# Optimization experiments

Hardware: AMD Instinct MI355X
Metric: run time of the kernel (lower is better)

## Reference

```python
import jax, jax.numpy as jnp
import numpy as np

B, V, FN, C = 8, 50000, 100000, 64


def setup_inputs() -> dict:
    key = jax.random.key(0)
    keys = iter(jax.random.split(key, 16))
    inp = {}
    inp["centers"] = jax.random.normal(next(keys), (B, 3, FN), jnp.float32)
    inp["verts"] = jax.random.normal(next(keys), (B, V, 3), jnp.float32)
    inp["faces"] = jax.random.randint(next(keys), (B, FN, 3), 0, V)

    def bn(p):
        inp[p + "g"] = jnp.ones((C,), jnp.float32)
        inp[p + "bt"] = jnp.zeros((C,), jnp.float32)
        inp[p + "m"] = jnp.zeros((C,), jnp.float32)
        inp[p + "v"] = jnp.ones((C,), jnp.float32)

    inp["cw1"] = jax.random.normal(next(keys), (C, 3), jnp.float32) * 0.1
    inp["cb1"] = jnp.zeros((C,), jnp.float32); bn("c1")
    inp["cw2"] = jax.random.normal(next(keys), (C, C), jnp.float32) * 0.1
    inp["cb2"] = jnp.zeros((C,), jnp.float32); bn("c2")
    inp["vw1"] = jax.random.normal(next(keys), (C, 6), jnp.float32) * 0.1
    inp["vb1"] = jnp.zeros((C,), jnp.float32); bn("v1")
    inp["vw2"] = jax.random.normal(next(keys), (C, C), jnp.float32) * 0.1
    inp["vb2"] = jnp.zeros((C,), jnp.float32); bn("v2")
    inp["sw"] = jax.random.normal(next(keys), (C, 2 * C), jnp.float32) * 0.1
    inp["sb"] = jnp.zeros((C,), jnp.float32); bn("s1")
    return inp


def _cbr(x, w, b, g, bt, m, v, eps=1e-5):
    # 1x1 Conv1d == pointwise GEMM over channel dim, then eval-mode BN, then ReLU
    y = jnp.einsum('bcf,oc->bof', x, w) + b[:, None]
    y = (y - m[:, None]) * (g[:, None] / jnp.sqrt(v[:, None] + eps)) + bt[:, None]
    return jax.nn.relu(y)


def _forward(faces, centers, verts,
             cw1, cb1, c1g, c1bt, c1m, c1v, cw2, cb2, c2g, c2bt, c2m, c2v,
             vw1, vb1, v1g, v1bt, v1m, v1v, vw2, vb2, v2g, v2bt, v2m, v2v,
             sw, sb, s1g, s1bt, s1m, s1v):
    Bb, Fn, _ = faces.shape
    # gather 3 corner vertices per face: [B, 3F, 3] -> [B, 9, F] (v0xyz, v1xyz, v2xyz)
    idx = faces.reshape(Bb, Fn * 3)
    corners = jnp.take_along_axis(verts, idx[:, :, None], axis=1)
    c9 = corners.reshape(Bb, Fn, 9).transpose(0, 2, 1)

    def vmlp(x):
        return _cbr(_cbr(x, vw1, vb1, v1g, v1bt, v1m, v1v), vw2, vb2, v2g, v2bt, v2m, v2v)

    vfeat = (vmlp(c9[:, :6])
             + vmlp(c9[:, 3:9])
             + vmlp(jnp.concatenate([c9[:, 6:9], c9[:, :3]], axis=1))) / 3.0
    cfeat = _cbr(_cbr(centers, cw1, cb1, c1g, c1bt, c1m, c1v), cw2, cb2, c2g, c2bt, c2m, c2v)
    return _cbr(jnp.concatenate([cfeat, vfeat], axis=1), sw, sb, s1g, s1bt, s1m, s1v)


def reference(centers, verts, faces,
              cw1, cb1, c1g, c1bt, c1m, c1v, cw2, cb2, c2g, c2bt, c2m, c2v,
              vw1, vb1, v1g, v1bt, v1m, v1v, vw2, vb2, v2g, v2bt, v2m, v2v,
              sw, sb, s1g, s1bt, s1m, s1v):
    return _forward(faces, centers, verts,
                    cw1, cb1, c1g, c1bt, c1m, c1v, cw2, cb2, c2g, c2bt, c2m, c2v,
                    vw1, vb1, v1g, v1bt, v1m, v1v, vw2, vb2, v2g, v2bt, v2m, v2v,
                    sw, sb, s1g, s1bt, s1m, s1v)
```

## Files before the change

### kernel.cpp

```cpp
#include <hip/hip_runtime.h>
#include <cstddef>
#include <cstdint>

#define FN_ 100000
#define V_  50000
#define B_  8
#define NT  128
#define NBLK (B_ * FN_ / NT)

#define WS_SHS 49152

typedef _Float16 f16;
typedef f16   f16x8 __attribute__((ext_vector_type(8)));
typedef float f32x4 __attribute__((ext_vector_type(4)));

struct Ptrs { const void* p[33]; };

union Pk4 { f16 h[4]; uint2 u; };
union Pk8 { f16 h[8]; uint4 u; };

__global__ __launch_bounds__(1024) void sd_prep(Ptrs in, f16* __restrict__ wsW,
                                                float* __restrict__ shsG)
{
  const float* __restrict__ cw1 = (const float*)in.p[3];
  const float* __restrict__ cb1 = (const float*)in.p[4];
  const float* __restrict__ c1g = (const float*)in.p[5];
  const float* __restrict__ c1bt= (const float*)in.p[6];
  const float* __restrict__ c1m = (const float*)in.p[7];
  const float* __restrict__ c1v = (const float*)in.p[8];
  const float* __restrict__ cw2 = (const float*)in.p[9];
  const float* __restrict__ cb2 = (const float*)in.p[10];
  const float* __restrict__ c2g = (const float*)in.p[11];
  const float* __restrict__ c2bt= (const float*)in.p[12];
  const float* __restrict__ c2m = (const float*)in.p[13];
  const float* __restrict__ c2v = (const float*)in.p[14];
  const float* __restrict__ vw1 = (const float*)in.p[15];
  const float* __restrict__ vb1 = (const float*)in.p[16];
  const float* __restrict__ v1g = (const float*)in.p[17];
  const float* __restrict__ v1bt= (const float*)in.p[18];
  const float* __restrict__ v1m = (const float*)in.p[19];
  const float* __restrict__ v1v = (const float*)in.p[20];
  const float* __restrict__ vw2 = (const float*)in.p[21];
  const float* __restrict__ vb2 = (const float*)in.p[22];
  const float* __restrict__ v2g = (const float*)in.p[23];
  const float* __restrict__ v2bt= (const float*)in.p[24];
  const float* __restrict__ v2m = (const float*)in.p[25];
  const float* __restrict__ v2v = (const float*)in.p[26];
  const float* __restrict__ sw  = (const float*)in.p[27];
  const float* __restrict__ sb  = (const float*)in.p[28];
  const float* __restrict__ s1g = (const float*)in.p[29];
  const float* __restrict__ s1bt= (const float*)in.p[30];
  const float* __restrict__ s1m = (const float*)in.p[31];
  const float* __restrict__ s1v = (const float*)in.p[32];

  __shared__ float scsL[448];
  const int tid = threadIdx.x;

  if (tid < 448) {
    const float *g, *v, *bb, *m, *bt; int o; float mul = 1.f;
    if (tid < 64)       { o = tid;      g=c1g; v=c1v; bb=cb1; m=c1m; bt=c1bt; }
    else if (tid < 256) { o = tid & 63; g=v1g; v=v1v; bb=vb1; m=v1m; bt=v1bt; }
    else if (tid < 320) { o = tid-256;  g=c2g; v=c2v; bb=cb2; m=c2m; bt=c2bt; }
    else if (tid < 384) { o = tid-320;  g=v2g; v=v2v; bb=vb2; m=v2m; bt=v2bt; mul = 1.f/3.f; }
    else                { o = tid-384;  g=s1g; v=s1v; bb=sb;  m=s1m; bt=s1bt; }
    float s = g[o] * rsqrtf(v[o] + 1e-5f);
    scsL[tid] = s * mul;
    shsG[tid] = ((bb[o] - m[o]) * s + bt[o]) * mul;
  }
  __syncthreads();

  for (int u = tid; u < 3072; u += 1024) {
    const int t = u >> 6, l = u & 63, r15 = l & 15, g4 = l >> 4;
    Pk8 pk;
    if (t < 16) {
      const int wm = t >> 2, tr = t & 3, row = 64*wm + 16*tr + r15;
#pragma unroll
      for (int j = 0; j < 8; ++j) {
        const int k = 8*g4 + j; float val = 0.f;
        if (wm == 0) { if (k >= 9 && k < 12) val = cw1[row*3 + (k-9)]; }
        else if (k < 9) {
          const int e = wm - 1, o = row - 64*wm, c = (k - 3*e + 9) % 9;
          if (c < 6) val = vw1[o*6 + c];
        }
        pk.h[j] = (f16)(val * scsL[row]);
      }
    } else if (t < 24) {
      const int tt = t-16, rt = tt >> 1, s = tt & 1, row = 16*rt + r15;
#pragma unroll
      for (int j = 0; j < 8; ++j) { const int k = 32*s + 8*g4 + j;
        pk.h[j] = (f16)(cw2[row*64 + k] * scsL[256+row]); }
    } else if (t < 32) {
      const int tt = t-24, rt = tt >> 1, s = tt & 1, row = 16*rt + r15;
#pragma unroll
      for (int j = 0; j < 8; ++j) { const int k = 32*s + 8*g4 + j;
        pk.h[j] = (f16)(vw2[row*64 + k] * scsL[320+row]); }
    } else {
      const int tt = t-32, rt = tt >> 2, s = tt & 3, row = 16*rt + r15;
#pragma unroll
      for (int j = 0; j < 8; ++j) { const int k = 32*s + 8*g4 + j;
        pk.h[j] = (f16)(sw[row*128 + k] * scsL[384+row]); }
    }
    *(uint4*)(wsW + (size_t)t*512 + l*8) = pk.u;
  }
}

__global__ __launch_bounds__(512, 4) void sd_main(const int* __restrict__ faces,
    const float* __restrict__ verts, const float* __restrict__ centers,
    const f16* __restrict__ wsW, const float* __restrict__ shsG,
    float* __restrict__ out)
{
  __shared__ f16 Hs[NT][296];
  __shared__ float shsL[448];

  const int tid  = threadIdx.x;
  const int lane = tid & 63;
  const int r15  = lane & 15;
  const int g4   = lane >> 4;
  const int wid  = __builtin_amdgcn_readfirstlane(tid >> 6);

  if (tid < 448) shsL[tid] = shsG[tid];

  {
    const int col = tid >> 2, p = tid & 3;
    const unsigned colg = blockIdx.x * (unsigned)NT + (unsigned)col;
    const unsigned b = colg / FN_;
    const unsigned f = colg - b * FN_;
    if (p < 3) {
      const int vi = faces[(size_t)colg*3 + p];
      const float* vp = verts + ((size_t)b*V_ + (size_t)vi)*3;
      Hs[col][256 + p*3 + 0] = (f16)vp[0];
      Hs[col][256 + p*3 + 1] = (f16)vp[1];
      Hs[col][256 + p*3 + 2] = (f16)vp[2];
    } else {
#pragma unroll
      for (int k = 0; k < 3; ++k)
        Hs[col][265 + k] = (f16)centers[((size_t)b*3 + k)*FN_ + f];
    }
#pragma unroll
    for (int z = 0; z < 5; ++z) Hs[col][268 + p*5 + z] = (f16)0.f;
  }
  __syncthreads();

  const int wm2 = wid >> 2, wn2 = wid & 3;

  f16x8 w2c[2][2], w2v[2][2];
#pragma unroll
  for (int tr = 0; tr < 2; ++tr)
#pragma unroll
    for (int s = 0; s < 2; ++s) {
      w2c[tr][s] = *(const f16x8*)(wsW + (size_t)(16 + (2*wm2+tr)*2 + s)*512 + lane*8);
      w2v[tr][s] = *(const f16x8*)(wsW + (size_t)(24 + (2*wm2+tr)*2 + s)*512 + lane*8);
    }

  {
    const int wm = wid >> 1, wn = wid & 1;
    f16x8 bfr[4];
#pragma unroll
    for (int tc = 0; tc < 4; ++tc)
      bfr[tc] = *(const f16x8*)&Hs[64*wn + 16*tc + r15][256 + 8*g4];
#pragma unroll
    for (int tr = 0; tr < 4; ++tr) {
      const f16x8 a = *(const f16x8*)(wsW + (size_t)(wm*4 + tr)*512 + lane*8);
#pragma unroll
      for (int tc = 0; tc < 4; ++tc) {
        f32x4 acc = {0.f,0.f,0.f,0.f};
        acc = __builtin_amdgcn_mfma_f32_16x16x32_f16(a, bfr[tc], acc, 0,0,0);
        const int o0  = 64*wm + 16*tr + 4*g4;
        const int col = 64*wn + 16*tc + r15;
        const f32x4 sh = *(const f32x4*)&shsL[o0];
        Pk4 pk;
#pragma unroll
        for (int j = 0; j < 4; ++j) pk.h[j] = (f16)fmaxf(acc[j] + sh[j], 0.f);
        *(uint2*)&Hs[col][o0] = pk.u;
      }
    }
  }
  __syncthreads();

  float cf[2][2][4], vf[2][2][4];
#pragma unroll
  for (int tr = 0; tr < 2; ++tr)
#pragma unroll
    for (int tc = 0; tc < 2; ++tc)
#pragma unroll
      for (int j = 0; j < 4; ++j) vf[tr][tc][j] = 0.f;

#pragma unroll
  for (int br = 0; br < 4; ++br) {
    f32x4 acc[2][2];
#pragma unroll
    for (int tr = 0; tr < 2; ++tr)
#pragma unroll
      for (int tc = 0; tc < 2; ++tc) acc[tr][tc] = (f32x4){0.f,0.f,0.f,0.f};
#pragma unroll
    for (int s = 0; s < 2; ++s) {
      const f16x8 b0 = *(const f16x8*)&Hs[32*wn2 +      r15][64*br + 32*s + 8*g4];
      const f16x8 b1 = *(const f16x8*)&Hs[32*wn2 + 16 + r15][64*br + 32*s + 8*g4];
#pragma unroll
      for (int tr = 0; tr < 2; ++tr) {
        const f16x8 a = br ? w2v[tr][s] : w2c[tr][s];
        acc[tr][0] = __builtin_amdgcn_mfma_f32_16x16x32_f16(a, b0, acc[tr][0], 0,0,0);
        acc[tr][1] = __builtin_amdgcn_mfma_f32_16x16x32_f16(a, b1, acc[tr][1], 0,0,0);
      }
    }
#pragma unroll
    for (int tr = 0; tr < 2; ++tr) {
      const int o0 = 32*wm2 + 16*tr + 4*g4;
      const f32x4 sh = br ? *(const f32x4*)&shsL[320+o0] : *(const f32x4*)&shsL[256+o0];
#pragma unroll
      for (int tc = 0; tc < 2; ++tc)
#pragma unroll
        for (int j = 0; j < 4; ++j) {
          if (br == 0) cf[tr][tc][j]  = fmaxf(acc[tr][tc][j] + sh[j], 0.f);
          else         vf[tr][tc][j] += fmaxf(acc[tr][tc][j] + sh[j], 0.f);
        }
    }
  }
  __syncthreads();

#pragma unroll
  for (int tr = 0; tr < 2; ++tr)
#pragma unroll
    for (int tc = 0; tc < 2; ++tc) {
      const int o0  = 32*wm2 + 16*tr + 4*g4;
      const int col = 32*wn2 + 16*tc + r15;
      Pk4 pc, pv;
#pragma unroll
      for (int j = 0; j < 4; ++j) { pc.h[j] = (f16)cf[tr][tc][j]; pv.h[j] = (f16)vf[tr][tc][j]; }
      *(uint2*)&Hs[col][o0]      = pc.u;
      *(uint2*)&Hs[col][64 + o0] = pv.u;
    }
  __syncthreads();

  {
    f32x4 acc[2][2];
#pragma unroll
    for (int tr = 0; tr < 2; ++tr)
#pragma unroll
      for (int tc = 0; tc < 2; ++tc) acc[tr][tc] = (f32x4){0.f,0.f,0.f,0.f};
#pragma unroll
    for (int s = 0; s < 4; ++s) {
      const f16x8 b0 = *(const f16x8*)&Hs[32*wn2 +      r15][32*s + 8*g4];
      const f16x8 b1 = *(const f16x8*)&Hs[32*wn2 + 16 + r15][32*s + 8*g4];
#pragma unroll
      for (int tr = 0; tr < 2; ++tr) {
        const f16x8 a = *(const f16x8*)(wsW + (size_t)(32 + (2*wm2+tr)*4 + s)*512 + lane*8);
        acc[tr][0] = __builtin_amdgcn_mfma_f32_16x16x32_f16(a, b0, acc[tr][0], 0,0,0);
        acc[tr][1] = __builtin_amdgcn_mfma_f32_16x16x32_f16(a, b1, acc[tr][1], 0,0,0);
      }
    }
#pragma unroll
    for (int tr = 0; tr < 2; ++tr)
#pragma unroll
      for (int tc = 0; tc < 2; ++tc) {
        const unsigned colg = blockIdx.x * (unsigned)NT + 32*wn2 + 16*tc + r15;
        const unsigned b = colg / FN_;
        const unsigned f = colg - b * FN_;
        const int o0 = 32*wm2 + 16*tr + 4*g4;
        const f32x4 sh = *(const f32x4*)&shsL[384 + o0];
#pragma unroll
        for (int j = 0; j < 4; ++j)
          out[((size_t)(b*64u + o0 + j))*FN_ + f] = fmaxf(acc[tr][tc][j] + sh[j], 0.f);
      }
  }
}

extern "C" void kernel_launch(void* const* d_in, const int* in_sizes, int n_in,
                              void* d_out, int out_size, void* d_ws, size_t ws_size,
                              hipStream_t stream) {
  (void)in_sizes; (void)n_in; (void)out_size; (void)ws_size;
  Ptrs p;
  for (int i = 0; i < 33; ++i) p.p[i] = d_in[i];
  f16*   wsW  = (f16*)d_ws;
  float* shsG = (float*)((char*)d_ws + WS_SHS);
  hipLaunchKernelGGL(sd_prep, dim3(1), dim3(1024), 0, stream, p, wsW, shsG);
  hipLaunchKernelGGL(sd_main, dim3(NBLK), dim3(512), 0, stream,
                     (const int*)d_in[2], (const float*)d_in[1], (const float*)d_in[0],
                     wsW, shsG, (float*)d_out);
}
```

Baseline: 98.02 us.

## Split layer-1 into two halves to shrink LDS tile and raise occupancy

Computes the first layer (64 centre channels plus 192 vertex channels) in two 128-row halves, each followed by its layer-2 GEMMs, so the shared-memory tile shrinks from 296 to 168 halves per column. Launch bounds rise to 6 waves per SIMD. The grid becomes 2D (face blocks by batch), which removes the per-column divide and handles the tail with bounds checks. Bias is folded into the MFMA accumulator init, and warps are remapped so each covers 16 rows by 64 columns. In exchange there are extra barriers and more register pressure from holding 4x4 accumulators.

```diff
diff --git a/kernel.cpp b/kernel.cpp
--- a/kernel.cpp
+++ b/kernel.cpp
@@ -6,7 +6,7 @@
 #define V_  50000
 #define B_  8
 #define NT  128
-#define NBLK (B_ * FN_ / NT)
+#define NBX 782
 
 #define WS_SHS 49152
 
@@ -104,12 +104,12 @@
   }
 }
 
-__global__ __launch_bounds__(512, 4) void sd_main(const int* __restrict__ faces,
+__global__ __launch_bounds__(512, 6) void sd_main(const int* __restrict__ faces,
     const float* __restrict__ verts, const float* __restrict__ centers,
     const f16* __restrict__ wsW, const float* __restrict__ shsG,
     float* __restrict__ out)
 {
-  __shared__ f16 Hs[NT][296];
+  __shared__ f16 Hs[NT][168];
   __shared__ float shsL[448];
 
   const int tid  = threadIdx.x;
@@ -117,151 +117,147 @@
   const int r15  = lane & 15;
   const int g4   = lane >> 4;
   const int wid  = __builtin_amdgcn_readfirstlane(tid >> 6);
+  const int rt   = wid & 3;
+  const int cg   = wid >> 2;
+
+  const int by   = blockIdx.y;
+  const int col0 = blockIdx.x * NT;
 
   if (tid < 448) shsL[tid] = shsG[tid];
 
   {
     const int col = tid >> 2, p = tid & 3;
-    const unsigned colg = blockIdx.x * (unsigned)NT + (unsigned)col;
-    const unsigned b = colg / FN_;
-    const unsigned f = colg - b * FN_;
+    const int f = col0 + col;
+    const bool valid = f < FN_;
     if (p < 3) {
-      const int vi = faces[(size_t)colg*3 + p];
-      const float* vp = verts + ((size_t)b*V_ + (size_t)vi)*3;
-      Hs[col][256 + p*3 + 0] = (f16)vp[0];
-      Hs[col][256 + p*3 + 1] = (f16)vp[1];
-      Hs[col][256 + p*3 + 2] = (f16)vp[2];
+      float x0 = 0.f, x1 = 0.f, x2 = 0.f;
+      if (valid) {
+        const int vi = faces[((size_t)by*FN_ + f)*3 + p];
+        const float* vp = verts + ((size_t)by*V_ + (size_t)vi)*3;
+        x0 = vp[0]; x1 = vp[1]; x2 = vp[2];
+      }
+      Hs[col][128 + p*3 + 0] = (f16)x0;
+      Hs[col][128 + p*3 + 1] = (f16)x1;
+      Hs[col][128 + p*3 + 2] = (f16)x2;
     } else {
 #pragma unroll
       for (int k = 0; k < 3; ++k)
-        Hs[col][265 + k] = (f16)centers[((size_t)b*3 + k)*FN_ + f];
-    }
-#pragma unroll
-    for (int z = 0; z < 5; ++z) Hs[col][268 + p*5 + z] = (f16)0.f;
+        Hs[col][137 + k] = valid ? (f16)centers[((size_t)by*3 + k)*FN_ + f] : (f16)0.f;
+    }
+#pragma unroll
+    for (int z = 0; z < 5; ++z) Hs[col][140 + p*5 + z] = (f16)0.f;
   }
   __syncthreads();
 
-  const int wm2 = wid >> 2, wn2 = wid & 3;
-
-  f16x8 w2c[2][2], w2v[2][2];
-#pragma unroll
-  for (int tr = 0; tr < 2; ++tr)
-#pragma unroll
-    for (int s = 0; s < 2; ++s) {
-      w2c[tr][s] = *(const f16x8*)(wsW + (size_t)(16 + (2*wm2+tr)*2 + s)*512 + lane*8);
-      w2v[tr][s] = *(const f16x8*)(wsW + (size_t)(24 + (2*wm2+tr)*2 + s)*512 + lane*8);
-    }
+  float cf[4][4], vf[4][4];
+  f16x8 w2v[2];
+
+#pragma unroll
+  for (int h = 0; h < 2; ++h) {
+    {
+      f16x8 bfr[4];
+#pragma unroll
+      for (int tc = 0; tc < 4; ++tc)
+        bfr[tc] = *(const f16x8*)&Hs[64*cg + 16*tc + r15][128 + 8*g4];
+#pragma unroll
+      for (int tr = 0; tr < 2; ++tr) {
+        const int t16 = 2*rt + tr;
+        const f16x8 a = *(const f16x8*)(wsW + (size_t)(8*h + t16)*512 + lane*8);
+        const f32x4 shv = *(const f32x4*)&shsL[128*h + t16*16 + 4*g4];
+#pragma unroll
+        for (int tc = 0; tc < 4; ++tc) {
+          f32x4 acc = shv;
+          acc = __builtin_amdgcn_mfma_f32_16x16x32_f16(a, bfr[tc], acc, 0,0,0);
+          Pk4 pk;
+#pragma unroll
+          for (int j = 0; j < 4; ++j) pk.h[j] = (f16)fmaxf(acc[j], 0.f);
+          *(uint2*)&Hs[64*cg + 16*tc + r15][t16*16 + 4*g4] = pk.u;
+        }
+      }
+    }
+    __syncthreads();
+
+#pragma unroll
+    for (int sub = 0; sub < 2; ++sub) {
+      const bool is_cf = (h == 0) && (sub == 0);
+      f16x8 wa[2];
+      if (is_cf) {
+#pragma unroll
+        for (int s = 0; s < 2; ++s)
+          wa[s] = *(const f16x8*)(wsW + (size_t)(16 + 2*rt + s)*512 + lane*8);
+      } else if (h == 0) {
+#pragma unroll
+        for (int s = 0; s < 2; ++s) {
+          w2v[s] = *(const f16x8*)(wsW + (size_t)(24 + 2*rt + s)*512 + lane*8);
+          wa[s] = w2v[s];
+        }
+      } else {
+#pragma unroll
+        for (int s = 0; s < 2; ++s) wa[s] = w2v[s];
+      }
+      const f32x4 shv = is_cf ? *(const f32x4*)&shsL[256 + rt*16 + 4*g4]
+                              : *(const f32x4*)&shsL[320 + rt*16 + 4*g4];
+      f32x4 acc[4];
+#pragma unroll
+      for (int tc = 0; tc < 4; ++tc) acc[tc] = shv;
+#pragma unroll
+      for (int s = 0; s < 2; ++s) {
+#pragma unroll
+        for (int tc = 0; tc < 4; ++tc) {
+          const f16x8 b = *(const f16x8*)&Hs[64*cg + 16*tc + r15][64*sub + 32*s + 8*g4];
+          acc[tc] = __builtin_amdgcn_mfma_f32_16x16x32_f16(wa[s], b, acc[tc], 0,0,0);
+        }
+      }
+#pragma unroll
+      for (int tc = 0; tc < 4; ++tc)
+#pragma unroll
+        for (int j = 0; j < 4; ++j) {
+          const float val = fmaxf(acc[tc][j], 0.f);
+          if (is_cf)       cf[tc][j]  = val;
+          else if (h == 0 && sub == 1) vf[tc][j]  = val;
+          else             vf[tc][j] += val;
+        }
+    }
+    __syncthreads();
+  }
+
+#pragma unroll
+  for (int tc = 0; tc < 4; ++tc) {
+    const int o0  = rt*16 + 4*g4;
+    const int col = 64*cg + 16*tc + r15;
+    Pk4 pc, pv;
+#pragma unroll
+    for (int j = 0; j < 4; ++j) { pc.h[j] = (f16)cf[tc][j]; pv.h[j] = (f16)vf[tc][j]; }
+    *(uint2*)&Hs[col][o0]      = pc.u;
+    *(uint2*)&Hs[col][64 + o0] = pv.u;
+  }
+  __syncthreads();
 
   {
-    const int wm = wid >> 1, wn = wid & 1;
-    f16x8 bfr[4];
-#pragma unroll
-    for (int tc = 0; tc < 4; ++tc)
-      bfr[tc] = *(const f16x8*)&Hs[64*wn + 16*tc + r15][256 + 8*g4];
-#pragma unroll
-    for (int tr = 0; tr < 4; ++tr) {
-      const f16x8 a = *(const f16x8*)(wsW + (size_t)(wm*4 + tr)*512 + lane*8);
+    const f32x4 shv = *(const f32x4*)&shsL[384 + rt*16 + 4*g4];
+    f32x4 acc[4];
+#pragma unroll
+    for (int tc = 0; tc < 4; ++tc) acc[tc] = shv;
+#pragma unroll
+    for (int s = 0; s < 4; ++s) {
+      const f16x8 a = *(const f16x8*)(wsW + (size_t)(32 + rt*4 + s)*512 + lane*8);
 #pragma unroll
       for (int tc = 0; tc < 4; ++tc) {
-        f32x4 acc = {0.f,0.f,0.f,0.f};
-        acc = __builtin_amdgcn_mfma_f32_16x16x32_f16(a, bfr[tc], acc, 0,0,0);
-        const int o0  = 64*wm + 16*tr + 4*g4;
-        const int col = 64*wn + 16*tc + r15;
-        const f32x4 sh = *(const f32x4*)&shsL[o0];
-        Pk4 pk;
-#pragma unroll
-        for (int j = 0; j < 4; ++j) pk.h[j] = (f16)fmaxf(acc[j] + sh[j], 0.f);
-        *(uint2*)&Hs[col][o0] = pk.u;
-      }
-    }
-  }
-  __syncthreads();
-
-  float cf[2][2][4], vf[2][2][4];
-#pragma unroll
-  for (int tr = 0; tr < 2; ++tr)
-#pragma unroll
-    for (int tc = 0; tc < 2; ++tc)
-#pragma unroll
-      for (int j = 0; j < 4; ++j) vf[tr][tc][j] = 0.f;
-
-#pragma unroll
-  for (int br = 0; br < 4; ++br) {
-    f32x4 acc[2][2];
-#pragma unroll
-    for (int tr = 0; tr < 2; ++tr)
-#pragma unroll
-      for (int tc = 0; tc < 2; ++tc) acc[tr][tc] = (f32x4){0.f,0.f,0.f,0.f};
-#pragma unroll
-    for (int s = 0; s < 2; ++s) {
-      const f16x8 b0 = *(const f16x8*)&Hs[32*wn2 +      r15][64*br + 32*s + 8*g4];
-      const f16x8 b1 = *(const f16x8*)&Hs[32*wn2 + 16 + r15][64*br + 32*s + 8*g4];
-#pragma unroll
-      for (int tr = 0; tr < 2; ++tr) {
-        const f16x8 a = br ? w2v[tr][s] : w2c[tr][s];
-        acc[tr][0] = __builtin_amdgcn_mfma_f32_16x16x32_f16(a, b0, acc[tr][0], 0,0,0);
-        acc[tr][1] = __builtin_amdgcn_mfma_f32_16x16x32_f16(a, b1, acc[tr][1], 0,0,0);
-      }
-    }
-#pragma unroll
-    for (int tr = 0; tr < 2; ++tr) {
-      const int o0 = 32*wm2 + 16*tr + 4*g4;
-      const f32x4 sh = br ? *(const f32x4*)&shsL[320+o0] : *(const f32x4*)&shsL[256+o0];
-#pragma unroll
-      for (int tc = 0; tc < 2; ++tc)
-#pragma unroll
-        for (int j = 0; j < 4; ++j) {
-          if (br == 0) cf[tr][tc][j]  = fmaxf(acc[tr][tc][j] + sh[j], 0.f);
-          else         vf[tr][tc][j] += fmaxf(acc[tr][tc][j] + sh[j], 0.f);
-        }
-    }
-  }
-  __syncthreads();
-
-#pragma unroll
-  for (int tr = 0; tr < 2; ++tr)
-#pragma unroll
-    for (int tc = 0; tc < 2; ++tc) {
-      const int o0  = 32*wm2 + 16*tr + 4*g4;
-      const int col = 32*wn2 + 16*tc + r15;
-      Pk4 pc, pv;
-#pragma unroll
-      for (int j = 0; j < 4; ++j) { pc.h[j] = (f16)cf[tr][tc][j]; pv.h[j] = (f16)vf[tr][tc][j]; }
-      *(uint2*)&Hs[col][o0]      = pc.u;
-      *(uint2*)&Hs[col][64 + o0] = pv.u;
-    }
-  __syncthreads();
-
-  {
-    f32x4 acc[2][2];
-#pragma unroll
-    for (int tr = 0; tr < 2; ++tr)
-#pragma unroll
-      for (int tc = 0; tc < 2; ++tc) acc[tr][tc] = (f32x4){0.f,0.f,0.f,0.f};
-#pragma unroll
-    for (int s = 0; s < 4; ++s) {
-      const f16x8 b0 = *(const f16x8*)&Hs[32*wn2 +      r15][32*s + 8*g4];
-      const f16x8 b1 = *(const f16x8*)&Hs[32*wn2 + 16 + r15][32*s + 8*g4];
-#pragma unroll
-      for (int tr = 0; tr < 2; ++tr) {
-        const f16x8 a = *(const f16x8*)(wsW + (size_t)(32 + (2*wm2+tr)*4 + s)*512 + lane*8);
-        acc[tr][0] = __builtin_amdgcn_mfma_f32_16x16x32_f16(a, b0, acc[tr][0], 0,0,0);
-        acc[tr][1] = __builtin_amdgcn_mfma_f32_16x16x32_f16(a, b1, acc[tr][1], 0,0,0);
-      }
-    }
-#pragma unroll
-    for (int tr = 0; tr < 2; ++tr)
-#pragma unroll
-      for (int tc = 0; tc < 2; ++tc) {
-        const unsigned colg = blockIdx.x * (unsigned)NT + 32*wn2 + 16*tc + r15;
-        const unsigned b = colg / FN_;
-        const unsigned f = colg - b * FN_;
-        const int o0 = 32*wm2 + 16*tr + 4*g4;
-        const f32x4 sh = *(const f32x4*)&shsL[384 + o0];
+        const f16x8 b = *(const f16x8*)&Hs[64*cg + 16*tc + r15][32*s + 8*g4];
+        acc[tc] = __builtin_amdgcn_mfma_f32_16x16x32_f16(a, b, acc[tc], 0,0,0);
+      }
+    }
+    const int o0 = rt*16 + 4*g4;
+#pragma unroll
+    for (int tc = 0; tc < 4; ++tc) {
+      const int f = col0 + 64*cg + 16*tc + r15;
+      if (f < FN_) {
+        const size_t base = ((size_t)(by*64 + o0))*FN_ + f;
 #pragma unroll
         for (int j = 0; j < 4; ++j)
-          out[((size_t)(b*64u + o0 + j))*FN_ + f] = fmaxf(acc[tr][tc][j] + sh[j], 0.f);
-      }
+          out[base + (size_t)j*FN_] = fmaxf(acc[tc][j], 0.f);
+      }
+    }
   }
 }
 
@@ -274,7 +270,7 @@
   f16*   wsW  = (f16*)d_ws;
   float* shsG = (float*)((char*)d_ws + WS_SHS);
   hipLaunchKernelGGL(sd_prep, dim3(1), dim3(1024), 0, stream, p, wsW, shsG);
-  hipLaunchKernelGGL(sd_main, dim3(NBLK), dim3(512), 0, stream,
+  hipLaunchKernelGGL(sd_main, dim3(NBX, B_), dim3(512), 0, stream,
                      (const int*)d_in[2], (const float*)d_in[1], (const float*)d_in[0],
                      wsW, shsG, (float*)d_out);
 }
```

Result: slower. 104.8 us (+7.0%).
